# Kernel tuning notes

Hardware: AMD Instinct MI355X
Metric: run time of the kernel (lower is better)

Reference implementation:

```python
import jax, jax.numpy as jnp
import numpy as np

NUM_ROUTING = 3

def squash(s):
    # squash along the unit_size axis (axis=2), exactly as the torch module
    mag_sq = jnp.sum(s * s, axis=2, keepdims=True)
    mag = jnp.sqrt(mag_sq)
    return mag_sq / (1.0 + mag_sq) * (s / mag)

def setup_inputs() -> dict:
    key = jax.random.key(0)
    k1, k2 = jax.random.split(key)
    B, in_unit, in_channel = 512, 8, 1152
    num_unit, unit_size = 10, 16
    x = jax.random.normal(k1, (B, in_unit, in_channel), dtype=jnp.float32)
    weight = jax.random.normal(k2, (in_channel, num_unit, unit_size, in_unit), dtype=jnp.float32)
    return {"x": x, "weight": weight}

def reference(x, weight):
    B = x.shape[0]
    C, J = weight.shape[0], weight.shape[1]  # in_channel, num_unit
    xt = jnp.swapaxes(x, 1, 2)  # [B, C, in_unit]
    # u_hat[c, j, b, s] = W[c, j, s, :] @ x[b, c, :]
    u_hat = jnp.einsum('cjsi,bci->cjbs', weight, xt)  # [C, J, B, S]
    b_ij = jnp.zeros((C, J), dtype=x.dtype)
    v = None
    for _ in range(NUM_ROUTING):
        # DGL degree-bucketing puts all J capsule nodes in one bucket, so the
        # softmax(dim=0) in capsule_reduce is over the num_unit axis per input capsule
        c = jax.nn.softmax(b_ij, axis=1)          # [C, J]
        s = jnp.einsum('cj,cjbs->jbs', c, u_hat)  # [J, B, S]
        v = squash(s)                             # [J, B, S]
        # update_edge: b_ij += mean over batch of <v_j, u_hat_ij>
        b_ij = b_ij + jnp.einsum('jbs,cjbs->cj', v, u_hat) / B
    # [J, B, S] -> [B, J, S] -> unsqueeze(1).unsqueeze(4).squeeze(1) -> [B, J, S, 1]
    return jnp.transpose(v, (1, 0, 2))[..., None]
```

## Files before the change

### kernel.cpp

```cpp
#include <hip/hip_runtime.h>
#include <math.h>

#define B_  512
#define I_  8
#define C_  1152
#define J_  10
#define S_  16
#define K1  9216
#define NKB 288
#define KBT 16

typedef short short8 __attribute__((ext_vector_type(8)));
typedef float floatx4 __attribute__((ext_vector_type(4)));

__device__ inline unsigned short f2bf(float f) {
    unsigned int u = __float_as_uint(f);
    return (unsigned short)((u + 0x7FFFu + ((u >> 16) & 1u)) >> 16);
}
__device__ inline unsigned int pack2(float a, float b) {
    return (unsigned int)f2bf(a) | ((unsigned int)f2bf(b) << 16);
}

__global__ __launch_bounds__(512) void k_pack(const float* __restrict__ x,
                                              const float* __restrict__ W,
                                              uint4* __restrict__ Bs,
                                              uint4* __restrict__ Bt,
                                              uint4* __restrict__ Wf,
                                              unsigned short* __restrict__ W2,
                                              float* __restrict__ b_ij) {
    __shared__ float lds[10240];
    const int task = blockIdx.x;
    const int t = threadIdx.x;
    const int w = t >> 6, L = t & 63, quad = L >> 4;

    if (task < 576) {
        const int bt = task / 36, kt = task % 36;
        const int b0 = bt * 32, k0 = kt * 256;
        #pragma unroll
        for (int p = 0; p < 4; p++) {
            int f4 = p * 512 + t;
            int row = f4 >> 6, c4 = (f4 & 63) << 2;
            *(float4*)&lds[row * 260 + c4] =
                *(const float4*)&x[(size_t)(b0 + row) * K1 + k0 + c4];
        }
        __syncthreads();
        #pragma unroll
        for (int p = 0; p < 2; p++) {
            const int bl = p * 16 + (L & 15);
            const float* s = &lds[bl * 260 + w * 32 + quad * 8];
            uint4 o;
            o.x = pack2(s[0], s[1]); o.y = pack2(s[2], s[3]);
            o.z = pack2(s[4], s[5]); o.w = pack2(s[6], s[7]);
            Bs[((size_t)(bt * 2 + p) * NKB + kt * 8 + w) * 64 + L] = o;
        }
        #pragma unroll
        for (int p = 0; p < 2; p++) {
            const int ntl = w * 2 + p;
            const int nl = ntl * 16 + (L & 15);
            float v[8];
            #pragma unroll
            for (int e = 0; e < 8; e++) v[e] = lds[(quad * 8 + e) * 260 + nl];
            uint4 o;
            o.x = pack2(v[0], v[1]); o.y = pack2(v[2], v[3]);
            o.z = pack2(v[4], v[5]); o.w = pack2(v[6], v[7]);
            Bt[((size_t)(kt * 16 + ntl) * KBT + bt) * 64 + L] = o;
        }
    } else if (task < 720) {
        const int c0 = (task - 576) * 8;
        #pragma unroll
        for (int p = 0; p < 5; p++) {
            int f4 = p * 512 + t;
            int cc = f4 / 320, off4 = (f4 % 320) << 2;
            *(float4*)&lds[cc * 1280 + off4] =
                *(const float4*)&W[(size_t)(c0 + cc) * 1280 + off4];
        }
        __syncthreads();
        #pragma unroll
        for (int p = 0; p < 3; p++) {
            int o = p * 512 + t;
            if (o < 1280) {
                int j = o >> 7, i = (o >> 4) & 7, m = o & 15;
                int k0w = i * C_ + c0;
                int Lw = m | (((k0w >> 3) & 3) << 4);
                float v[8];
                #pragma unroll
                for (int e = 0; e < 8; e++)
                    v[e] = lds[e * 1280 + j * 128 + m * 8 + i];
                uint4 og;
                og.x = pack2(v[0], v[1]); og.y = pack2(v[2], v[3]);
                og.z = pack2(v[4], v[5]); og.w = pack2(v[6], v[7]);
                Wf[((size_t)j * NKB + (k0w >> 5)) * 64 + Lw] = og;
            }
        }
        #pragma unroll
        for (int p = 0; p < 2; p++) {
            int o = p * 512 + t;
            if (o < 640) {
                int j = o >> 6, i = (o >> 3) & 7, cc = o & 7;
                unsigned int r8[8];
                #pragma unroll
                for (int h = 0; h < 8; h++)
                    r8[h] = pack2(lds[cc * 1280 + j * 128 + (2 * h) * 8 + i],
                                  lds[cc * 1280 + j * 128 + (2 * h + 1) * 8 + i]);
                unsigned short* dst = W2 + ((size_t)(j * 8 + i) * C_ + c0 + cc) * 16;
                *(uint4*)dst       = make_uint4(r8[0], r8[1], r8[2], r8[3]);
                *(uint4*)(dst + 8) = make_uint4(r8[4], r8[5], r8[6], r8[7]);
            }
        }
    } else {
        for (int idx = t; idx < C_ * J_; idx += 512) b_ij[idx] = 0.0f;
    }
}

__global__ __launch_bounds__(512) void k_sgemm_f(const short8* __restrict__ Wf,
                                                 const short8* __restrict__ Bs,
                                                 const float* __restrict__ b_ij,
                                                 unsigned short* __restrict__ Vf,
                                                 float* __restrict__ out,
                                                 int mode) {
    __shared__ float smf[1152 + 4096];
    const int t = threadIdx.x, w = t >> 6, L = t & 63, quad = L >> 4;
    const int j = blockIdx.x >> 4;
    const int ntp = blockIdx.x & 15;

    if (mode) {
        for (int c = t; c < C_; c += 512) {
            float bv[J_], mx = -1e30f;
            #pragma unroll
            for (int jj = 0; jj < J_; jj++) {
                bv[jj] = b_ij[c * J_ + jj]; mx = fmaxf(mx, bv[jj]);
            }
            float sum = 0.0f;
            #pragma unroll
            for (int jj = 0; jj < J_; jj++) sum += __expf(bv[jj] - mx);
            smf[c] = __expf(bv[j] - mx) / sum;
        }
    }
    __syncthreads();

    const short8* pA  = Wf + ((size_t)j * NKB + w * 36) * 64 + L;
    const short8* pB0 = Bs + ((size_t)(ntp * 2) * NKB + w * 36) * 64 + L;
    const short8* pB1 = pB0 + (size_t)NKB * 64;
    floatx4 c0 = {0.f, 0.f, 0.f, 0.f}, c1 = c0;

    if (mode) {
        #pragma unroll 4
        for (int i = 0; i < 36; i++) {
            short8 a = pA[i * 64];
            const int cb = i * 32 + quad * 8;
            float4 cl = *(const float4*)&smf[cb];
            float4 ch = *(const float4*)&smf[cb + 4];
            float cn8[8] = {cl.x, cl.y, cl.z, cl.w, ch.x, ch.y, ch.z, ch.w};
            unsigned int* au = (unsigned int*)&a;
            short8 a2; unsigned int* ao = (unsigned int*)&a2;
            #pragma unroll
            for (int h = 0; h < 4; h++) {
                float f0 = __uint_as_float(au[h] << 16)         * cn8[2 * h];
                float f1 = __uint_as_float(au[h] & 0xffff0000u) * cn8[2 * h + 1];
                ao[h] = pack2(f0, f1);
            }
            c0 = __builtin_amdgcn_mfma_f32_16x16x32_bf16(a2, pB0[i * 64], c0, 0, 0, 0);
            c1 = __builtin_amdgcn_mfma_f32_16x16x32_bf16(a2, pB1[i * 64], c1, 0, 0, 0);
        }
    } else {
        #pragma unroll 4
        for (int i = 0; i < 36; i++) {
            short8 a = pA[i * 64];
            c0 = __builtin_amdgcn_mfma_f32_16x16x32_bf16(a, pB0[i * 64], c0, 0, 0, 0);
            c1 = __builtin_amdgcn_mfma_f32_16x16x32_bf16(a, pB1[i * 64], c1, 0, 0, 0);
        }
    }

    const int col = L & 15, rw = quad << 2;
    float* base = &smf[1152 + w * 512];
    #pragma unroll
    for (int r = 0; r < 4; r++) {
        base[      (rw + r) * 16 + col] = c0[r];
        base[256 + (rw + r) * 16 + col] = c1[r];
    }
    __syncthreads();

    if (t < 32) {
        const int ntl = t >> 4, bl = t & 15;
        float sv[S_]; float msq = 0.f;
        #pragma unroll
        for (int s = 0; s < S_; s++) {
            float a = 0.f;
            #pragma unroll
            for (int w8 = 0; w8 < 8; w8++)
                a += smf[1152 + w8 * 512 + ntl * 256 + s * 16 + bl];
            if (mode == 0) a *= 0.1f;
            sv[s] = a; msq += a * a;
        }
        const float scale = msq / ((1.f + msq) * sqrtf(msq));
        const int b = ntp * 32 + t;
        if (mode < 2) {
            const int kb = b >> 5, lh = (b >> 3) & 3, e = b & 7;
            #pragma unroll
            for (int s = 0; s < S_; s++)
                Vf[((size_t)(j * KBT + kb) * 64 + (s | (lh << 4))) * 8 + e] =
                    f2bf(sv[s] * scale);
        } else {
            float o16[S_];
            #pragma unroll
            for (int s = 0; s < S_; s++) o16[s] = sv[s] * scale;
            float* dst = &out[((size_t)b * J_ + j) * S_];
            #pragma unroll
            for (int r4 = 0; r4 < 4; r4++)
                *(float4*)(dst + r4 * 4) = *(float4*)(o16 + r4 * 4);
        }
    }
}

__global__ __launch_bounds__(512) void k_tgemm_bup(const short8* __restrict__ Vf,
                                                   const short8* __restrict__ Bt,
                                                   const unsigned short* __restrict__ W2,
                                                   float* __restrict__ b_ij) {
    const int t = threadIdx.x, w = t >> 6, L = t & 63;
    const int j = blockIdx.y, ntg = blockIdx.x;
    const int nt = ntg * 8 + w;
    const short8* pA = Vf + (size_t)j * KBT * 64 + L;
    const short8* pB = Bt + (size_t)nt * KBT * 64 + L;
    floatx4 a = {0.f, 0.f, 0.f, 0.f};
    #pragma unroll
    for (int kb = 0; kb < KBT; kb++)
        a = __builtin_amdgcn_mfma_f32_16x16x32_bf16(pA[kb * 64], pB[kb * 64], a, 0, 0, 0);
    const int col = L & 15, rw = (L >> 4) << 2;
    const int i = nt / 72;
    const int c = (nt % 72) * 16 + col;
    const unsigned short* wp = W2 + ((size_t)(j * 8 + i) * C_ + c) * 16 + rw;
    uint2 wv = *(const uint2*)wp;
    float p = a[0] * __uint_as_float((unsigned int)wv.x << 16)
            + a[1] * __uint_as_float(wv.x & 0xffff0000u)
            + a[2] * __uint_as_float((unsigned int)wv.y << 16)
            + a[3] * __uint_as_float(wv.y & 0xffff0000u);
    p += __shfl_xor(p, 16);
    p += __shfl_xor(p, 32);
    if ((L >> 4) == 0)
        atomicAdd(&b_ij[c * J_ + j], p * (1.0f / 512.f));
}

extern "C" void kernel_launch(void* const* d_in, const int* in_sizes, int n_in,
                              void* d_out, int out_size, void* d_ws, size_t ws_size,
                              hipStream_t stream) {
    const float* x = (const float*)d_in[0];
    const float* W = (const float*)d_in[1];
    float* out = (float*)d_out;
    float* ws  = (float*)d_ws;

    float* Bs_f = ws;
    float* Bt_f = Bs_f + 2359296;
    float* Wf_f = Bt_f + 2359296;
    float* W2_f = Wf_f + 737280;
    float* Vf_f = W2_f + 737280;
    float* bij  = Vf_f + 40960;

    k_pack<<<721, 512, 0, stream>>>(x, W, (uint4*)Bs_f, (uint4*)Bt_f,
                                    (uint4*)Wf_f, (unsigned short*)W2_f, bij);

    k_sgemm_f<<<160, 512, 0, stream>>>((const short8*)Wf_f, (const short8*)Bs_f,
                                       bij, (unsigned short*)Vf_f, out, 0);
    k_tgemm_bup<<<dim3(72, 10), 512, 0, stream>>>(
        (const short8*)Vf_f, (const short8*)Bt_f, (const unsigned short*)W2_f, bij);

    k_sgemm_f<<<160, 512, 0, stream>>>((const short8*)Wf_f, (const short8*)Bs_f,
                                       bij, (unsigned short*)Vf_f, out, 1);
    k_tgemm_bup<<<dim3(72, 10), 512, 0, stream>>>(
        (const short8*)Vf_f, (const short8*)Bt_f, (const unsigned short*)W2_f, bij);

    k_sgemm_f<<<160, 512, 0, stream>>>((const short8*)Wf_f, (const short8*)Bs_f,
                                       bij, (unsigned short*)Vf_f, out, 2);
}
```

Before: 143.0 us.

## Fuse s-GEMM and b-update GEMM into one kernel with per-capsule spin flags

Merges each routing iteration's squash GEMM and agreement GEMM into a single launch. Producer blocks write V via atomic stores and bump a per-j done counter, while consumer blocks spin on that counter and then accumulate into a separate b buffer. Carrying the previous b into the new buffer avoids an in-place read/write hazard. The aim is to remove two kernel launches and the gaps between them. This relies on all producer blocks being scheduled before consumers starve them, and uses a bounded spin as a safety valve.

```diff
diff --git a/kernel.cpp b/kernel.cpp
--- a/kernel.cpp
+++ b/kernel.cpp
@@ -27,7 +27,9 @@
                                               uint4* __restrict__ Bt,
                                               uint4* __restrict__ Wf,
                                               unsigned short* __restrict__ W2,
-                                              float* __restrict__ b_ij) {
+                                              float* __restrict__ b1,
+                                              float* __restrict__ b2,
+                                              int* __restrict__ done) {
     __shared__ float lds[10240];
     const int task = blockIdx.x;
     const int t = threadIdx.x;
@@ -108,33 +110,172 @@
             }
         }
     } else {
-        for (int idx = t; idx < C_ * J_; idx += 512) b_ij[idx] = 0.0f;
-    }
-}
-
-__global__ __launch_bounds__(512) void k_sgemm_f(const short8* __restrict__ Wf,
-                                                 const short8* __restrict__ Bs,
-                                                 const float* __restrict__ b_ij,
-                                                 unsigned short* __restrict__ Vf,
-                                                 float* __restrict__ out,
-                                                 int mode) {
+        for (int idx = t; idx < C_ * J_; idx += 512) { b1[idx] = 0.0f; b2[idx] = 0.0f; }
+        if (t < 32) done[t] = 0;
+    }
+}
+
+__global__ __launch_bounds__(512, 8) void k_iter(
+    const short8* __restrict__ Wf, const short8* __restrict__ Bs,
+    const short8* __restrict__ Bt, const unsigned short* __restrict__ W2,
+    const float* __restrict__ b_in, float* __restrict__ b_out,
+    unsigned int* __restrict__ Vf_dw, int* __restrict__ done, int uniform)
+{
+    __shared__ float smf[5760];
+    unsigned int* smu = (unsigned int*)smf;
+    const int t = threadIdx.x, w = t >> 6, L = t & 63, quad = L >> 4;
+    const int bx = blockIdx.x;
+
+    if (bx < 160) {
+        const int j = bx >> 4, ntp = bx & 15;
+        if (!uniform) {
+            for (int c = t; c < C_; c += 512) {
+                float bv[J_], mx = -1e30f;
+                #pragma unroll
+                for (int jj = 0; jj < J_; jj++) {
+                    bv[jj] = b_in[c * J_ + jj]; mx = fmaxf(mx, bv[jj]);
+                }
+                float sum = 0.0f;
+                #pragma unroll
+                for (int jj = 0; jj < J_; jj++) sum += __expf(bv[jj] - mx);
+                smf[c] = __expf(bv[j] - mx) / sum;
+            }
+        }
+        __syncthreads();
+
+        const short8* pA  = Wf + ((size_t)j * NKB + w * 36) * 64 + L;
+        const short8* pB0 = Bs + ((size_t)(ntp * 2) * NKB + w * 36) * 64 + L;
+        const short8* pB1 = pB0 + (size_t)NKB * 64;
+        floatx4 c0 = {0.f, 0.f, 0.f, 0.f}, c1 = c0;
+        if (!uniform) {
+            #pragma unroll 4
+            for (int i = 0; i < 36; i++) {
+                short8 a = pA[i * 64];
+                const int cb = i * 32 + quad * 8;
+                float4 cl = *(const float4*)&smf[cb];
+                float4 ch = *(const float4*)&smf[cb + 4];
+                float cn8[8] = {cl.x, cl.y, cl.z, cl.w, ch.x, ch.y, ch.z, ch.w};
+                unsigned int* au = (unsigned int*)&a;
+                short8 a2; unsigned int* ao = (unsigned int*)&a2;
+                #pragma unroll
+                for (int h = 0; h < 4; h++) {
+                    float f0 = __uint_as_float(au[h] << 16)         * cn8[2 * h];
+                    float f1 = __uint_as_float(au[h] & 0xffff0000u) * cn8[2 * h + 1];
+                    ao[h] = pack2(f0, f1);
+                }
+                c0 = __builtin_amdgcn_mfma_f32_16x16x32_bf16(a2, pB0[i * 64], c0, 0, 0, 0);
+                c1 = __builtin_amdgcn_mfma_f32_16x16x32_bf16(a2, pB1[i * 64], c1, 0, 0, 0);
+            }
+        } else {
+            #pragma unroll 4
+            for (int i = 0; i < 36; i++) {
+                short8 a = pA[i * 64];
+                c0 = __builtin_amdgcn_mfma_f32_16x16x32_bf16(a, pB0[i * 64], c0, 0, 0, 0);
+                c1 = __builtin_amdgcn_mfma_f32_16x16x32_bf16(a, pB1[i * 64], c1, 0, 0, 0);
+            }
+        }
+        const int col = L & 15, rw = quad << 2;
+        float* base = &smf[1152 + w * 512];
+        #pragma unroll
+        for (int r = 0; r < 4; r++) {
+            base[      (rw + r) * 16 + col] = c0[r];
+            base[256 + (rw + r) * 16 + col] = c1[r];
+        }
+        __syncthreads();
+        if (t < 32) {
+            const int ntl = t >> 4, bl = t & 15;
+            float sv[S_]; float msq = 0.f;
+            #pragma unroll
+            for (int s = 0; s < S_; s++) {
+                float a = 0.f;
+                #pragma unroll
+                for (int w8 = 0; w8 < 8; w8++)
+                    a += smf[1152 + w8 * 512 + ntl * 256 + s * 16 + bl];
+                if (uniform) a *= 0.1f;
+                sv[s] = a; msq += a * a;
+            }
+            const float scale = msq / ((1.f + msq) * sqrtf(msq));
+            #pragma unroll
+            for (int s = 0; s < S_; s++)
+                smf[5248 + t * 16 + s] = sv[s] * scale;
+        }
+        __syncthreads();
+        if (t < 16) {
+            const int lh = t >> 2, ew = t & 3;
+            #pragma unroll
+            for (int s = 0; s < S_; s++) {
+                unsigned int d = pack2(smf[5248 + (2 * t) * 16 + s],
+                                       smf[5248 + (2 * t + 1) * 16 + s]);
+                int dw = ((j * 16 + ntp) * 64 + (s | (lh << 4))) * 4 + ew;
+                __hip_atomic_store(&Vf_dw[dw], d,
+                                   __ATOMIC_RELAXED, __HIP_MEMORY_SCOPE_AGENT);
+            }
+        }
+        __syncthreads();
+        if (t == 0)
+            __hip_atomic_fetch_add(&done[j], 1,
+                                   __ATOMIC_RELAXED, __HIP_MEMORY_SCOPE_AGENT);
+    } else {
+        const int tb = bx - 160;
+        const int j = tb / 72, ntg = tb % 72;
+        if (t == 0) {
+            int spins = 0;
+            while (__hip_atomic_load(&done[j], __ATOMIC_RELAXED,
+                                     __HIP_MEMORY_SCOPE_AGENT) < 16) {
+                __builtin_amdgcn_s_sleep(1);
+                if (++spins > (1 << 22)) break;
+            }
+        }
+        __syncthreads();
+        for (int d = t; d < 4096; d += 512)
+            smu[d] = __hip_atomic_load(&Vf_dw[j * 4096 + d],
+                                       __ATOMIC_RELAXED, __HIP_MEMORY_SCOPE_AGENT);
+        __syncthreads();
+        const int nt = ntg * 8 + w;
+        const short8* pA = (const short8*)smu + L;
+        const short8* pB = Bt + (size_t)nt * KBT * 64 + L;
+        floatx4 a = {0.f, 0.f, 0.f, 0.f};
+        #pragma unroll
+        for (int kb = 0; kb < KBT; kb++)
+            a = __builtin_amdgcn_mfma_f32_16x16x32_bf16(pA[kb * 64], pB[kb * 64], a, 0, 0, 0);
+        const int col = L & 15, rw = (L >> 4) << 2;
+        const int i = nt / 72;
+        const int c = (nt % 72) * 16 + col;
+        const unsigned short* wp = W2 + ((size_t)(j * 8 + i) * C_ + c) * 16 + rw;
+        uint2 wv = *(const uint2*)wp;
+        float p = a[0] * __uint_as_float((unsigned int)wv.x << 16)
+                + a[1] * __uint_as_float(wv.x & 0xffff0000u)
+                + a[2] * __uint_as_float((unsigned int)wv.y << 16)
+                + a[3] * __uint_as_float(wv.y & 0xffff0000u);
+        p += __shfl_xor(p, 16);
+        p += __shfl_xor(p, 32);
+        if ((L >> 4) == 0) {
+            float add = p * (1.0f / 512.f);
+            if (i == 0 && !uniform) add += b_in[c * J_ + j];
+            atomicAdd(&b_out[c * J_ + j], add);
+        }
+    }
+}
+
+__global__ __launch_bounds__(512) void k_sgemm_out(const short8* __restrict__ Wf,
+                                                   const short8* __restrict__ Bs,
+                                                   const float* __restrict__ b_ij,
+                                                   float* __restrict__ out) {
     __shared__ float smf[1152 + 4096];
     const int t = threadIdx.x, w = t >> 6, L = t & 63, quad = L >> 4;
     const int j = blockIdx.x >> 4;
     const int ntp = blockIdx.x & 15;
 
-    if (mode) {
-        for (int c = t; c < C_; c += 512) {
-            float bv[J_], mx = -1e30f;
-            #pragma unroll
-            for (int jj = 0; jj < J_; jj++) {
-                bv[jj] = b_ij[c * J_ + jj]; mx = fmaxf(mx, bv[jj]);
-            }
-            float sum = 0.0f;
-            #pragma unroll
-            for (int jj = 0; jj < J_; jj++) sum += __expf(bv[jj] - mx);
-            smf[c] = __expf(bv[j] - mx) / sum;
-        }
+    for (int c = t; c < C_; c += 512) {
+        float bv[J_], mx = -1e30f;
+        #pragma unroll
+        for (int jj = 0; jj < J_; jj++) {
+            bv[jj] = b_ij[c * J_ + jj]; mx = fmaxf(mx, bv[jj]);
+        }
+        float sum = 0.0f;
+        #pragma unroll
+        for (int jj = 0; jj < J_; jj++) sum += __expf(bv[jj] - mx);
+        smf[c] = __expf(bv[j] - mx) / sum;
     }
     __syncthreads();
 
@@ -142,35 +283,24 @@
     const short8* pB0 = Bs + ((size_t)(ntp * 2) * NKB + w * 36) * 64 + L;
     const short8* pB1 = pB0 + (size_t)NKB * 64;
     floatx4 c0 = {0.f, 0.f, 0.f, 0.f}, c1 = c0;
-
-    if (mode) {
-        #pragma unroll 4
-        for (int i = 0; i < 36; i++) {
-            short8 a = pA[i * 64];
-            const int cb = i * 32 + quad * 8;
-            float4 cl = *(const float4*)&smf[cb];
-            float4 ch = *(const float4*)&smf[cb + 4];
-            float cn8[8] = {cl.x, cl.y, cl.z, cl.w, ch.x, ch.y, ch.z, ch.w};
-            unsigned int* au = (unsigned int*)&a;
-            short8 a2; unsigned int* ao = (unsigned int*)&a2;
-            #pragma unroll
-            for (int h = 0; h < 4; h++) {
-                float f0 = __uint_as_float(au[h] << 16)         * cn8[2 * h];
-                float f1 = __uint_as_float(au[h] & 0xffff0000u) * cn8[2 * h + 1];
-                ao[h] = pack2(f0, f1);
-            }
-            c0 = __builtin_amdgcn_mfma_f32_16x16x32_bf16(a2, pB0[i * 64], c0, 0, 0, 0);
-            c1 = __builtin_amdgcn_mfma_f32_16x16x32_bf16(a2, pB1[i * 64], c1, 0, 0, 0);
-        }
-    } else {
-        #pragma unroll 4
-        for (int i = 0; i < 36; i++) {
-            short8 a = pA[i * 64];
-            c0 = __builtin_amdgcn_mfma_f32_16x16x32_bf16(a, pB0[i * 64], c0, 0, 0, 0);
-            c1 = __builtin_amdgcn_mfma_f32_16x16x32_bf16(a, pB1[i * 64], c1, 0, 0, 0);
-        }
-    }
-
+    #pragma unroll 4
+    for (int i = 0; i < 36; i++) {
+        short8 a = pA[i * 64];
+        const int cb = i * 32 + quad * 8;
+        float4 cl = *(const float4*)&smf[cb];
+        float4 ch = *(const float4*)&smf[cb + 4];
+        float cn8[8] = {cl.x, cl.y, cl.z, cl.w, ch.x, ch.y, ch.z, ch.w};
+        unsigned int* au = (unsigned int*)&a;
+        short8 a2; unsigned int* ao = (unsigned int*)&a2;
+        #pragma unroll
+        for (int h = 0; h < 4; h++) {
+            float f0 = __uint_as_float(au[h] << 16)         * cn8[2 * h];
+            float f1 = __uint_as_float(au[h] & 0xffff0000u) * cn8[2 * h + 1];
+            ao[h] = pack2(f0, f1);
+        }
+        c0 = __builtin_amdgcn_mfma_f32_16x16x32_bf16(a2, pB0[i * 64], c0, 0, 0, 0);
+        c1 = __builtin_amdgcn_mfma_f32_16x16x32_bf16(a2, pB1[i * 64], c1, 0, 0, 0);
+    }
     const int col = L & 15, rw = quad << 2;
     float* base = &smf[1152 + w * 512];
     #pragma unroll
@@ -179,7 +309,6 @@
         base[256 + (rw + r) * 16 + col] = c1[r];
     }
     __syncthreads();
-
     if (t < 32) {
         const int ntl = t >> 4, bl = t & 15;
         float sv[S_]; float msq = 0.f;
@@ -189,55 +318,18 @@
             #pragma unroll
             for (int w8 = 0; w8 < 8; w8++)
                 a += smf[1152 + w8 * 512 + ntl * 256 + s * 16 + bl];
-            if (mode == 0) a *= 0.1f;
             sv[s] = a; msq += a * a;
         }
         const float scale = msq / ((1.f + msq) * sqrtf(msq));
         const int b = ntp * 32 + t;
-        if (mode < 2) {
-            const int kb = b >> 5, lh = (b >> 3) & 3, e = b & 7;
-            #pragma unroll
-            for (int s = 0; s < S_; s++)
-                Vf[((size_t)(j * KBT + kb) * 64 + (s | (lh << 4))) * 8 + e] =
-                    f2bf(sv[s] * scale);
-        } else {
-            float o16[S_];
-            #pragma unroll
-            for (int s = 0; s < S_; s++) o16[s] = sv[s] * scale;
-            float* dst = &out[((size_t)b * J_ + j) * S_];
-            #pragma unroll
-            for (int r4 = 0; r4 < 4; r4++)
-                *(float4*)(dst + r4 * 4) = *(float4*)(o16 + r4 * 4);
-        }
-    }
-}
-
-__global__ __launch_bounds__(512) void k_tgemm_bup(const short8* __restrict__ Vf,
-                                                   const short8* __restrict__ Bt,
-                                                   const unsigned short* __restrict__ W2,
-                                                   float* __restrict__ b_ij) {
-    const int t = threadIdx.x, w = t >> 6, L = t & 63;
-    const int j = blockIdx.y, ntg = blockIdx.x;
-    const int nt = ntg * 8 + w;
-    const short8* pA = Vf + (size_t)j * KBT * 64 + L;
-    const short8* pB = Bt + (size_t)nt * KBT * 64 + L;
-    floatx4 a = {0.f, 0.f, 0.f, 0.f};
-    #pragma unroll
-    for (int kb = 0; kb < KBT; kb++)
-        a = __builtin_amdgcn_mfma_f32_16x16x32_bf16(pA[kb * 64], pB[kb * 64], a, 0, 0, 0);
-    const int col = L & 15, rw = (L >> 4) << 2;
-    const int i = nt / 72;
-    const int c = (nt % 72) * 16 + col;
-    const unsigned short* wp = W2 + ((size_t)(j * 8 + i) * C_ + c) * 16 + rw;
-    uint2 wv = *(const uint2*)wp;
-    float p = a[0] * __uint_as_float((unsigned int)wv.x << 16)
-            + a[1] * __uint_as_float(wv.x & 0xffff0000u)
-            + a[2] * __uint_as_float((unsigned int)wv.y << 16)
-            + a[3] * __uint_as_float(wv.y & 0xffff0000u);
-    p += __shfl_xor(p, 16);
-    p += __shfl_xor(p, 32);
-    if ((L >> 4) == 0)
-        atomicAdd(&b_ij[c * J_ + j], p * (1.0f / 512.f));
+        float o16[S_];
+        #pragma unroll
+        for (int s = 0; s < S_; s++) o16[s] = sv[s] * scale;
+        float* dst = &out[((size_t)b * J_ + j) * S_];
+        #pragma unroll
+        for (int r4 = 0; r4 < 4; r4++)
+            *(float4*)(dst + r4 * 4) = *(float4*)(o16 + r4 * 4);
+    }
 }
 
 extern "C" void kernel_launch(void* const* d_in, const int* in_sizes, int n_in,
@@ -253,21 +345,20 @@
     float* Wf_f = Bt_f + 2359296;
     float* W2_f = Wf_f + 737280;
     float* Vf_f = W2_f + 737280;
-    float* bij  = Vf_f + 40960;
+    float* b1   = Vf_f + 40960;
+    float* b2   = b1 + 11520;
+    int*   done = (int*)(b2 + 11520);
 
     k_pack<<<721, 512, 0, stream>>>(x, W, (uint4*)Bs_f, (uint4*)Bt_f,
-                                    (uint4*)Wf_f, (unsigned short*)W2_f, bij);
-
-    k_sgemm_f<<<160, 512, 0, stream>>>((const short8*)Wf_f, (const short8*)Bs_f,
-                                       bij, (unsigned short*)Vf_f, out, 0);
-    k_tgemm_bup<<<dim3(72, 10), 512, 0, stream>>>(
-        (const short8*)Vf_f, (const short8*)Bt_f, (const unsigned short*)W2_f, bij);
-
-    k_sgemm_f<<<160, 512, 0, stream>>>((const short8*)Wf_f, (const short8*)Bs_f,
-                                       bij, (unsigned short*)Vf_f, out, 1);
-    k_tgemm_bup<<<dim3(72, 10), 512, 0, stream>>>(
-        (const short8*)Vf_f, (const short8*)Bt_f, (const unsigned short*)W2_f, bij);
-
-    k_sgemm_f<<<160, 512, 0, stream>>>((const short8*)Wf_f, (const short8*)Bs_f,
-                                       bij, (unsigned short*)Vf_f, out, 2);
-}
+                                    (uint4*)Wf_f, (unsigned short*)W2_f,
+                                    b1, b2, done);
+
+    k_iter<<<880, 512, 0, stream>>>((const short8*)Wf_f, (const short8*)Bs_f,
+                                    (const short8*)Bt_f, (const unsigned short*)W2_f,
+                                    b1, b1, (unsigned int*)Vf_f, done, 1);
+    k_iter<<<880, 512, 0, stream>>>((const short8*)Wf_f, (const short8*)Bs_f,
+                                    (const short8*)Bt_f, (const unsigned short*)W2_f,
+                                    b1, b2, (unsigned int*)Vf_f, done + 16, 0);
+    k_sgemm_out<<<160, 512, 0, stream>>>((const short8*)Wf_f, (const short8*)Bs_f,
+                                         b2, out);
+}
```

After: 171.8 us. +20.1%, slower.
